# Kernel tuning notes

Hardware: AMD Instinct MI355X
Metric: run time of the kernel (lower is better)

The kernel has to match this reference:

```python
import jax, jax.numpy as jnp
import numpy as np
import math

D_MODEL = 1024
NHEAD = 16
HEAD_DIM = D_MODEL // NHEAD
D_FF = 4 * D_MODEL
EPS = 1e-5


def _layer_norm(x, g, b):
    mu = jnp.mean(x, axis=-1, keepdims=True)
    var = jnp.mean(jnp.square(x - mu), axis=-1, keepdims=True)
    return (x - mu) * jax.lax.rsqrt(var + EPS) * g + b


def setup_inputs() -> dict:
    key = jax.random.key(0)
    ks = jax.random.split(key, 12)
    B, N = 2, 2048
    s = 1.0 / math.sqrt(D_MODEL)
    inp = {
        "x": jax.random.normal(ks[0], (B, N, D_MODEL), dtype=jnp.float32),
        "wq": jax.random.normal(ks[1], (D_MODEL, D_MODEL), dtype=jnp.float32) * s,
        "bq": jnp.zeros((D_MODEL,), jnp.float32),
        "wk": jax.random.normal(ks[2], (D_MODEL, D_MODEL), dtype=jnp.float32) * s,
        "bk": jnp.zeros((D_MODEL,), jnp.float32),
        "wv": jax.random.normal(ks[3], (D_MODEL, D_MODEL), dtype=jnp.float32) * s,
        "bv": jnp.zeros((D_MODEL,), jnp.float32),
        "wo": jax.random.normal(ks[4], (D_MODEL, D_MODEL), dtype=jnp.float32) * s,
        "bo": jnp.zeros((D_MODEL,), jnp.float32),
        "ln1_g": jnp.ones((D_MODEL,), jnp.float32),
        "ln1_b": jnp.zeros((D_MODEL,), jnp.float32),
        "ln2_g": jnp.ones((D_MODEL,), jnp.float32),
        "ln2_b": jnp.zeros((D_MODEL,), jnp.float32),
        "w1": jax.random.normal(ks[5], (D_MODEL, D_FF), dtype=jnp.float32) * s,
        "b1": jnp.zeros((D_FF,), jnp.float32),
        "w2": jax.random.normal(ks[6], (D_FF, D_MODEL), dtype=jnp.float32) * (1.0 / math.sqrt(D_FF)),
        "b2": jnp.zeros((D_MODEL,), jnp.float32),
    }
    return inp


def reference(x, wq, bq, wk, bk, wv, bv, wo, bo, ln1_g, ln1_b, ln2_g, ln2_b, w1, b1, w2, b2):
    B, N, _ = x.shape
    normed = _layer_norm(x, ln1_g, ln1_b)
    # projections -> [B, H, N, Dh]
    q = (normed @ wq + bq).reshape(B, N, NHEAD, HEAD_DIM).transpose(0, 2, 1, 3)
    k = (normed @ wk + bk).reshape(B, N, NHEAD, HEAD_DIM).transpose(0, 2, 1, 3)
    v = (normed @ wv + bv).reshape(B, N, NHEAD, HEAD_DIM).transpose(0, 2, 1, 3)
    raw_scores = jnp.einsum("bhqd,bhkd->bhqk", q, k) / math.sqrt(HEAD_DIM)
    attn_probs = jax.nn.sigmoid(raw_scores)
    attn_out = jnp.einsum("bhqk,bhkd->bhqd", attn_probs, v) / math.sqrt(N)
    attn_out = attn_out.transpose(0, 2, 1, 3).reshape(B, N, D_MODEL)
    x = x + (attn_out @ wo + bo)  # dropout is identity in eval
    normed2 = _layer_norm(x, ln2_g, ln2_b)
    ff = jax.nn.gelu(normed2 @ w1 + b1, approximate=False) @ w2 + b2
    x = x + ff
    return (x, attn_probs)
```

## Files before the change

kernel.cpp:

```cpp
#include <hip/hip_runtime.h>
#include <hip/hip_bf16.h>
#include <math.h>

#define DMODEL 1024
#define NSEQ   2048
#define NBATCH 2
#define NHEADS 16
#define DHEAD  64
#define DFF    4096
#define MROWS  (NBATCH*NSEQ)
#define QKVLD  3072

typedef __attribute__((ext_vector_type(8))) short bf16x8;
typedef __attribute__((ext_vector_type(4))) float f32x4;

static __device__ __forceinline__ ushort f2b(float f) {
    return __builtin_bit_cast(ushort, (__bf16)f);
}

static __device__ __forceinline__ f32x4 mfma16(bf16x8 a, bf16x8 b, f32x4 c) {
    return __builtin_amdgcn_mfma_f32_16x16x32_bf16(a, b, c, 0, 0, 0);
}

static __device__ __forceinline__ void gload_lds16(const void* g, void* lds) {
    __builtin_amdgcn_global_load_lds((const __attribute__((address_space(1))) void*)g,
                                     (__attribute__((address_space(3))) void*)lds,
                                     16, 0, 0);
}

static __device__ __forceinline__ void softbar() {
    __builtin_amdgcn_sched_barrier(0);
    asm volatile("s_waitcnt lgkmcnt(0)" ::: "memory");
    __builtin_amdgcn_s_barrier();
    __builtin_amdgcn_sched_barrier(0);
}

static __device__ __forceinline__ void cast_tile_lds(const float* __restrict__ W,
                                                     ushort* __restrict__ Wt,
                                                     int K, int Nn, int bx, int by, int t,
                                                     float (*lds)[65])
{
    const int n0 = bx * 64;
    const int k0 = by * 64;
#pragma unroll
    for (int r = 0; r < 4; ++r) {
        const int kr = (t >> 4) + r * 16;
        const int nc = (t & 15) * 4;
        const float4 v = *(const float4*)(W + (long)(k0 + kr) * Nn + n0 + nc);
        lds[kr][nc] = v.x; lds[kr][nc + 1] = v.y; lds[kr][nc + 2] = v.z; lds[kr][nc + 3] = v.w;
    }
    __syncthreads();
    const int n  = t >> 2;
    const int kc = (t & 3) * 16;
    ushort tmp[16];
#pragma unroll
    for (int i = 0; i < 16; ++i) tmp[i] = f2b(lds[kc + i][n]);
    *(uint4*)(Wt + (long)(n0 + n) * K + k0 + kc)     = *(const uint4*)tmp;
    *(uint4*)(Wt + (long)(n0 + n) * K + k0 + kc + 8) = *(const uint4*)(tmp + 8);
}

__global__ __launch_bounds__(256) void prep(const float* __restrict__ wq,
                                            const float* __restrict__ wk,
                                            const float* __restrict__ wv,
                                            const float* __restrict__ wo,
                                            const float* __restrict__ w1,
                                            const float* __restrict__ w2,
                                            const float* __restrict__ bq,
                                            const float* __restrict__ bk,
                                            const float* __restrict__ bv,
                                            const float* __restrict__ x,
                                            const float* __restrict__ ln1g,
                                            const float* __restrict__ ln1b,
                                            ushort* __restrict__ wqkv_t,
                                            ushort* __restrict__ wo_t,
                                            ushort* __restrict__ w1_t,
                                            ushort* __restrict__ w2_t,
                                            float* __restrict__ bqkv,
                                            ushort* __restrict__ normed)
{
    __shared__ float red[4];
    __shared__ float tl[64][65];
    const int id  = blockIdx.x;
    const int tid = threadIdx.x;

    if (id < 256) {
        cast_tile_lds(wq, wqkv_t, 1024, 1024, id & 15, id >> 4, tid, tl);
    } else if (id < 512) {
        const int i2 = id - 256;
        cast_tile_lds(wk, wqkv_t + 1024 * 1024, 1024, 1024, i2 & 15, i2 >> 4, tid, tl);
    } else if (id < 768) {
        const int i2 = id - 512;
        cast_tile_lds(wv, wqkv_t + 2048 * 1024, 1024, 1024, i2 & 15, i2 >> 4, tid, tl);
    } else if (id < 1024) {
        const int i2 = id - 768;
        cast_tile_lds(wo, wo_t, 1024, 1024, i2 & 15, i2 >> 4, tid, tl);
    } else if (id < 2048) {
        const int i2 = id - 1024;
        cast_tile_lds(w1, w1_t, 1024, 4096, i2 & 63, i2 >> 6, tid, tl);
    } else if (id < 3072) {
        const int i2 = id - 2048;
        cast_tile_lds(w2, w2_t, 4096, 1024, i2 & 15, i2 >> 4, tid, tl);
    } else if (id < 3088) {
        const int t = (id - 3072) * 256 + tid;
        float v = 0.0f;
        if (t < 1024)      v = bq[t];
        else if (t < 2048) v = bk[t - 1024];
        else if (t < 3072) v = bv[t - 2048];
        bqkv[t] = v;
    } else {
        const int row = id - 3088;
        const float4 v = ((const float4*)(x + (long)row * DMODEL))[tid];
        float s = v.x + v.y + v.z + v.w;
#pragma unroll
        for (int o = 32; o; o >>= 1) s += __shfl_down(s, o, 64);
        if ((tid & 63) == 0) red[tid >> 6] = s;
        __syncthreads();
        const float mu = (red[0] + red[1] + red[2] + red[3]) * (1.0f / DMODEL);
        __syncthreads();
        const float d0 = v.x - mu, d1 = v.y - mu, d2 = v.z - mu, d3 = v.w - mu;
        float s2 = d0*d0 + d1*d1 + d2*d2 + d3*d3;
#pragma unroll
        for (int o = 32; o; o >>= 1) s2 += __shfl_down(s2, o, 64);
        if ((tid & 63) == 0) red[tid >> 6] = s2;
        __syncthreads();
        const float inv = rsqrtf((red[0] + red[1] + red[2] + red[3]) * (1.0f / DMODEL) + 1e-5f);
        const float4 gg = ((const float4*)ln1g)[tid];
        const float4 bv4 = ((const float4*)ln1b)[tid];
        ushort4 o4;
        o4.x = f2b(d0 * inv * gg.x + bv4.x);
        o4.y = f2b(d1 * inv * gg.y + bv4.y);
        o4.z = f2b(d2 * inv * gg.z + bv4.z);
        o4.w = f2b(d3 * inv * gg.w + bv4.w);
        ((ushort4*)(normed + (long)row * DMODEL))[tid] = o4;
    }
}

__global__ __launch_bounds__(256) void ln_kernel(const float* __restrict__ x,
                                                 const float* __restrict__ g,
                                                 const float* __restrict__ bb,
                                                 ushort* __restrict__ out)
{
    const int row = blockIdx.x;
    const int tid = threadIdx.x;
    const float4 v = ((const float4*)(x + (long)row * DMODEL))[tid];
    float s = v.x + v.y + v.z + v.w;
#pragma unroll
    for (int o = 32; o; o >>= 1) s += __shfl_down(s, o, 64);
    __shared__ float red[4];
    if ((tid & 63) == 0) red[tid >> 6] = s;
    __syncthreads();
    const float mu = (red[0] + red[1] + red[2] + red[3]) * (1.0f / DMODEL);
    __syncthreads();
    const float d0 = v.x - mu, d1 = v.y - mu, d2 = v.z - mu, d3 = v.w - mu;
    float s2 = d0*d0 + d1*d1 + d2*d2 + d3*d3;
#pragma unroll
    for (int o = 32; o; o >>= 1) s2 += __shfl_down(s2, o, 64);
    if ((tid & 63) == 0) red[tid >> 6] = s2;
    __syncthreads();
    const float inv = rsqrtf((red[0] + red[1] + red[2] + red[3]) * (1.0f / DMODEL) + 1e-5f);
    const float4 gg = ((const float4*)g)[tid];
    const float4 bv = ((const float4*)bb)[tid];
    ushort4 o4;
    o4.x = f2b(d0 * inv * gg.x + bv.x);
    o4.y = f2b(d1 * inv * gg.y + bv.y);
    o4.z = f2b(d2 * inv * gg.z + bv.z);
    o4.w = f2b(d3 * inv * gg.w + bv.w);
    ((ushort4*)(out + (long)row * DMODEL))[tid] = o4;
}

template<bool GELU>
__global__ __launch_bounds__(512, 2) void gemm128(const ushort* __restrict__ A, int lda,
                                                  const ushort* __restrict__ Bt, int ldb,
                                                  const float* __restrict__ bias,
                                                  ushort* __restrict__ C, int ldc, int K)
{
    extern __shared__ char smem[];
    const int tid  = threadIdx.x;
    const int lane = tid & 63;
    const int w    = tid >> 6;
    const int wm   = w >> 2;
    const int wn   = w & 3;
    const long row0 = (long)blockIdx.x * 128;
    const long col0 = (long)blockIdx.y * 256;

    const int srow = tid >> 2;
    const int scol = (((tid & 3) ^ ((srow >> 1) & 3))) * 8;
    const ushort* Ag = A  + (row0 + srow) * (long)lda + scol;
    const ushort* Bg = Bt + (col0 + srow) * (long)ldb + scol;

#define STAGE_A1(buf, k0)                                                                  \
    gload_lds16(Ag + (k0), smem + (buf) * 8192 + w * 1024)
#define STAGE_B1(buf, k0)                                                                  \
    do {                                                                                   \
        gload_lds16(Bg + (k0),                   smem + 24576 + (buf) * 16384 + w * 1024); \
        gload_lds16(Bg + 128 * (long)ldb + (k0), smem + 24576 + (buf) * 16384 + 8192 + w * 1024); \
    } while (0)

    const f32x4 zero = {0.f, 0.f, 0.f, 0.f};
    f32x4 acc[4][4];
#pragma unroll
    for (int m = 0; m < 4; ++m)
#pragma unroll
        for (int j = 0; j < 4; ++j) acc[m][j] = zero;

    const int NT = K >> 5;
    STAGE_A1(0, 0);  STAGE_B1(0, 0);
    STAGE_A1(1, 32); STAGE_B1(1, 32);

    const int mrow = lane & 15;
    const int xsl  = (((lane >> 4) ^ ((mrow >> 1) & 3))) * 8;
    const int abase = (wm * 64 + mrow) * 32 + xsl;
    const int bbase = (wn * 64 + mrow) * 32 + xsl;

    for (int t = 0; t < NT; ++t) {
        if (t == NT - 1) asm volatile("s_waitcnt vmcnt(0)" ::: "memory");
        else             asm volatile("s_waitcnt vmcnt(3)" ::: "memory");
        __builtin_amdgcn_sched_barrier(0);
        __builtin_amdgcn_s_barrier();
        __builtin_amdgcn_sched_barrier(0);

        const int cb = t % 3;
        const ushort* Abase = (const ushort*)(smem + cb * 8192);
        const ushort* Bbase = (const ushort*)(smem + 24576 + cb * 16384);

        bf16x8 bfr[4], afr[2];
#pragma unroll
        for (int ni = 0; ni < 4; ++ni)
            bfr[ni] = *(const bf16x8*)&Bbase[bbase + ni * 512];
#pragma unroll
        for (int mi = 0; mi < 2; ++mi)
            afr[mi] = *(const bf16x8*)&Abase[abase + mi * 512];
        if (t + 2 < NT) STAGE_A1((t + 2) % 3, (t + 2) * 32);
        __builtin_amdgcn_s_setprio(1);
#pragma unroll
        for (int mi = 0; mi < 2; ++mi)
#pragma unroll
            for (int ni = 0; ni < 4; ++ni)
                acc[mi][ni] = mfma16(afr[mi], bfr[ni], acc[mi][ni]);
        __builtin_amdgcn_s_setprio(0);

#pragma unroll
        for (int mi = 0; mi < 2; ++mi)
            afr[mi] = *(const bf16x8*)&Abase[abase + (mi + 2) * 512];
        if (t + 2 < NT) STAGE_B1((t + 2) % 3, (t + 2) * 32);
        __builtin_amdgcn_s_setprio(1);
#pragma unroll
        for (int mi = 0; mi < 2; ++mi)
#pragma unroll
            for (int ni = 0; ni < 4; ++ni)
                acc[mi + 2][ni] = mfma16(afr[mi], bfr[ni], acc[mi + 2][ni]);
        __builtin_amdgcn_s_setprio(0);
    }
#undef STAGE_A1
#undef STAGE_B1

#pragma unroll
    for (int ni = 0; ni < 4; ++ni) {
        const int colg = (int)col0 + wn * 64 + ni * 16 + (lane & 15);
        const float bcol = bias[colg];
#pragma unroll
        for (int mi = 0; mi < 4; ++mi) {
#pragma unroll
            for (int r = 0; r < 4; ++r) {
                const long rowg = row0 + wm * 64 + mi * 16 + (lane >> 4) * 4 + r;
                float vv = acc[mi][ni][r] + bcol;
                if (GELU) vv = 0.5f * vv * (1.0f + erff(vv * 0.70710678118f));
                C[rowg * ldc + colg] = f2b(vv);
            }
        }
    }
}

template<bool OUTF32, bool GELU, bool RES, bool NTST>
__global__ __launch_bounds__(512, 2) void gemm4s(const ushort* __restrict__ A, int lda,
                                                 const ushort* __restrict__ Bt, int ldb,
                                                 const float* __restrict__ bias,
                                                 const float* __restrict__ res,
                                                 void* __restrict__ Cout,
                                                 int Nn, int K)
{
    extern __shared__ char smem[];
    const int tid  = threadIdx.x;
    const int lane = tid & 63;
    const int g    = tid >> 8;
    const int tg   = tid & 255;
    const int w4   = tg >> 6;
    const int wm   = w4 >> 1, wn = w4 & 1;
    const long row0 = (long)blockIdx.x * 128;
    const long col0 = (long)blockIdx.y * 128;
    const int mrow = lane & 15;
    const int xsl  = (((lane >> 4) ^ ((mrow >> 1) & 3))) * 8;

    const int srow = tg >> 2;
    const int soff = (((tg & 3) ^ ((srow >> 1) & 3))) * 8;
    const int kb   = g * (K >> 1);
    const ushort* Ag = A  + (row0 + srow) * (long)lda + kb + soff;
    const ushort* Bg = Bt + (col0 + srow) * (long)ldb + kb + soff;
    char* Als = smem + g * 32768;
    char* Bls = smem + 65536 + g * 32768;

#define STAGE4S(buf, k0)                                                          \
    do {                                                                          \
        gload_lds16(Ag + (k0),                  Als + ((buf) << 13) + w4 * 1024); \
        gload_lds16(Ag + 64 * (long)lda + (k0), Als + ((buf) << 13) + 4096 + w4 * 1024); \
        gload_lds16(Bg + (k0),                  Bls + ((buf) << 13) + w4 * 1024); \
        gload_lds16(Bg + 64 * (long)ldb + (k0), Bls + ((buf) << 13) + 4096 + w4 * 1024); \
    } while (0)

    const f32x4 zero = {0.f, 0.f, 0.f, 0.f};
    f32x4 acc[4][4];
#pragma unroll
    for (int m = 0; m < 4; ++m)
#pragma unroll
        for (int j = 0; j < 4; ++j) acc[m][j] = zero;

    const int NT2 = K >> 6;
    STAGE4S(0, 0);
    STAGE4S(1, 32);
    STAGE4S(2, 64);

    const int abase = (wm * 64 + mrow) * 32 + xsl;
    const int bbase = (wn * 64 + mrow) * 32 + xsl;

    for (int t = 0; t < NT2; ++t) {
        if      (t >= NT2 - 1) asm volatile("s_waitcnt vmcnt(0)" ::: "memory");
        else if (t == NT2 - 2) asm volatile("s_waitcnt vmcnt(4)" ::: "memory");
        else                   asm volatile("s_waitcnt vmcnt(8)" ::: "memory");
        __builtin_amdgcn_sched_barrier(0);
        __builtin_amdgcn_s_barrier();
        __builtin_amdgcn_sched_barrier(0);

        if (t + 3 < NT2) STAGE4S((t + 3) & 3, (t + 3) * 32);

        const ushort* Abase = (const ushort*)(Als + ((t & 3) << 13));
        const ushort* Bbase = (const ushort*)(Bls + ((t & 3) << 13));
        bf16x8 af[4], bfv[4];
#pragma unroll
        for (int m = 0; m < 4; ++m)
            af[m] = *(const bf16x8*)&Abase[abase + m * 512];
#pragma unroll
        for (int j = 0; j < 4; ++j)
            bfv[j] = *(const bf16x8*)&Bbase[bbase + j * 512];
        __builtin_amdgcn_s_setprio(1);
#pragma unroll
        for (int m = 0; m < 4; ++m)
#pragma unroll
            for (int j = 0; j < 4; ++j)
                acc[m][j] = mfma16(af[m], bfv[j], acc[m][j]);
        __builtin_amdgcn_s_setprio(0);
    }
#undef STAGE4S

    __syncthreads();
    float* xch = (float*)smem;
    if (g == 1) {
#pragma unroll
        for (int m = 0; m < 4; ++m)
#pragma unroll
            for (int j = 0; j < 4; ++j)
#pragma unroll
                for (int r = 0; r < 4; ++r)
                    xch[(m * 16 + j * 4 + r) * 256 + tg] = acc[m][j][r];
    }
    __syncthreads();
    if (g == 0) {
#pragma unroll
        for (int j = 0; j < 4; ++j) {
            const int colg  = (int)col0 + wn * 64 + j * 16 + mrow;
            const float bcol = bias[colg];
#pragma unroll
            for (int m = 0; m < 4; ++m) {
#pragma unroll
                for (int r = 0; r < 4; ++r) {
                    const long rowg = row0 + wm * 64 + m * 16 + (lane >> 4) * 4 + r;
                    float vv = acc[m][j][r] + xch[(m * 16 + j * 4 + r) * 256 + tg] + bcol;
                    if (RES)   vv += res[rowg * Nn + colg];
                    if (GELU)  vv = 0.5f * vv * (1.0f + erff(vv * 0.70710678118f));
                    if (OUTF32) {
                        if (NTST) __builtin_nontemporal_store(vv, (float*)Cout + rowg * Nn + colg);
                        else      ((float*)Cout)[rowg * Nn + colg] = vv;
                    } else {
                        ((ushort*)Cout)[rowg * Nn + colg] = f2b(vv);
                    }
                }
            }
        }
    }
}

__global__ __launch_bounds__(256) void transpose_v(const ushort* __restrict__ v,
                                                   ushort* __restrict__ vt)
{
    __shared__ ushort t[64][72];
    const int nb = blockIdx.x, bh = blockIdx.y, b = bh >> 4;
    const int hcol = (bh & 15) * DHEAD;
    const int tid  = threadIdx.x;
    const int rrow = tid >> 3;
    const int cch  = (tid & 7) * 8;
#pragma unroll
    for (int r = 0; r < 2; ++r) {
        const int nr = rrow + r * 32;
        *(uint4*)&t[nr][cch] =
            *(const uint4*)(v + ((long)(b * NSEQ + nb * 64 + nr)) * QKVLD + hcol + cch);
    }
    __syncthreads();
#pragma unroll
    for (int r = 0; r < 2; ++r) {
        const int d = rrow + r * 32;
        ushort tmp[8];
#pragma unroll
        for (int i = 0; i < 8; ++i) tmp[i] = t[cch + i][d];
        *(uint4*)(vt + ((long)bh * DHEAD + d) * NSEQ + nb * 64 + cch) = *(const uint4*)tmp;
    }
}

__global__ __launch_bounds__(256) void attn_kernel(const ushort* __restrict__ qkv,
                                                   const ushort* __restrict__ vt,
                                                   float* __restrict__ probs,
                                                   ushort* __restrict__ ao)
{
    __shared__ ushort Ks[64][72];
    __shared__ ushort Vs[64][72];
    __shared__ __align__(16) float Pf[4][16][68];
    const int tid  = threadIdx.x;
    const int lane = tid & 63;
    const int w    = tid >> 6;
    const int qb   = blockIdx.x;
    const int bh   = blockIdx.y;
    const int b    = bh >> 4;
    const int q0   = qb * 64 + w * 16;
    const int mrow = lane & 15;
    const int kof  = (lane >> 4) * 8;
    const int hcol = (bh & 15) * DHEAD;
    const int NT   = NSEQ / 64;

    bf16x8 aq0, aq1;
    {
        const ushort* qp = qkv + ((long)(b * NSEQ + q0 + mrow)) * QKVLD + hcol;
        aq0 = *(const bf16x8*)(qp + kof);
        aq1 = *(const bf16x8*)(qp + 32 + kof);
    }

    const f32x4 zero = {0.f, 0.f, 0.f, 0.f};
    f32x4 acco[4];
#pragma unroll
    for (int dj = 0; dj < 4; ++dj) acco[dj] = zero;

    const int srow = tid >> 3;
    const int sch  = (tid & 7) * 8;
    const ushort* km = qkv + 1024;

    uint4 kr0, kr1, vr0, vr1;
#define LOADT(kt)                                                                          \
    do {                                                                                   \
        kr0 = *(const uint4*)(km + ((long)(b * NSEQ + (kt) * 64 + srow)) * QKVLD + hcol + sch);       \
        kr1 = *(const uint4*)(km + ((long)(b * NSEQ + (kt) * 64 + srow + 32)) * QKVLD + hcol + sch);  \
        vr0 = *(const uint4*)(vt + ((long)bh * DHEAD + srow) * NSEQ + (kt) * 64 + sch);               \
        vr1 = *(const uint4*)(vt + ((long)bh * DHEAD + srow + 32) * NSEQ + (kt) * 64 + sch);          \
    } while (0)

    LOADT(0);

    for (int kt = 0; kt < NT; ++kt) {
        *(uint4*)&Ks[srow][sch]      = kr0;
        *(uint4*)&Ks[srow + 32][sch] = kr1;
        *(uint4*)&Vs[srow][sch]      = vr0;
        *(uint4*)&Vs[srow + 32][sch] = vr1;
        softbar();
        if (kt + 1 < NT) LOADT(kt + 1);

        f32x4 s[4];
#pragma unroll
        for (int j = 0; j < 4; ++j) s[j] = zero;
#pragma unroll
        for (int j = 0; j < 4; ++j) {
            bf16x8 b0 = *(const bf16x8*)&Ks[j * 16 + mrow][kof];
            bf16x8 b1 = *(const bf16x8*)&Ks[j * 16 + mrow][32 + kof];
            s[j] = mfma16(aq0, b0, s[j]);
            s[j] = mfma16(aq1, b1, s[j]);
        }

#pragma unroll
        for (int j = 0; j < 4; ++j) {
#pragma unroll
            for (int r = 0; r < 4; ++r) {
                const int rr = (lane >> 4) * 4 + r;
                const float e  = __expf(-0.125f * s[j][r]);
                const float pv = __builtin_amdgcn_rcpf(1.0f + e);
                Pf[w][rr][j * 16 + mrow] = pv;
            }
        }

        const long pbase = ((long)(bh * NSEQ + q0)) * NSEQ + kt * 64;
#pragma unroll
        for (int i = 0; i < 4; ++i) {
            const int rr = (lane >> 4) + 4 * i;
            const f32x4 pv4 = *(const f32x4*)&Pf[w][rr][mrow * 4];
            __builtin_nontemporal_store(pv4, (f32x4*)(probs + pbase + (long)rr * NSEQ + mrow * 4));
        }

#pragma unroll
        for (int ks = 0; ks < 2; ++ks) {
            const f32x4 f0 = *(const f32x4*)&Pf[w][mrow][ks * 32 + kof];
            const f32x4 f1 = *(const f32x4*)&Pf[w][mrow][ks * 32 + kof + 4];
            bf16x8 ap;
            ap[0] = (short)f2b(f0[0]); ap[1] = (short)f2b(f0[1]);
            ap[2] = (short)f2b(f0[2]); ap[3] = (short)f2b(f0[3]);
            ap[4] = (short)f2b(f1[0]); ap[5] = (short)f2b(f1[1]);
            ap[6] = (short)f2b(f1[2]); ap[7] = (short)f2b(f1[3]);
#pragma unroll
            for (int dj = 0; dj < 4; ++dj) {
                bf16x8 bv = *(const bf16x8*)&Vs[dj * 16 + mrow][ks * 32 + kof];
                acco[dj] = mfma16(ap, bv, acco[dj]);
            }
        }
        softbar();
    }
#undef LOADT

    const float sc = rsqrtf((float)NSEQ);
#pragma unroll
    for (int dj = 0; dj < 4; ++dj)
#pragma unroll
        for (int r = 0; r < 4; ++r) {
            const int rr = (lane >> 4) * 4 + r;
            ao[((long)(b * NSEQ + q0 + rr)) * DMODEL + hcol + dj * 16 + mrow] =
                f2b(acco[dj][r] * sc);
        }
}

extern "C" void kernel_launch(void* const* d_in, const int* in_sizes, int n_in,
                              void* d_out, int out_size, void* d_ws, size_t ws_size,
                              hipStream_t stream) {
    (void)in_sizes; (void)n_in; (void)out_size;
    const float* x    = (const float*)d_in[0];
    const float* wq   = (const float*)d_in[1];
    const float* bq   = (const float*)d_in[2];
    const float* wk   = (const float*)d_in[3];
    const float* bk   = (const float*)d_in[4];
    const float* wv   = (const float*)d_in[5];
    const float* bv   = (const float*)d_in[6];
    const float* wo   = (const float*)d_in[7];
    const float* bo   = (const float*)d_in[8];
    const float* ln1g = (const float*)d_in[9];
    const float* ln1b = (const float*)d_in[10];
    const float* ln2g = (const float*)d_in[11];
    const float* ln2b = (const float*)d_in[12];
    const float* w1   = (const float*)d_in[13];
    const float* b1   = (const float*)d_in[14];
    const float* w2   = (const float*)d_in[15];
    const float* b2   = (const float*)d_in[16];

    char* ws = (char*)d_ws;
    const size_t MB = 1u << 20;
    ushort* wqkv_t  = (ushort*)(ws + 0 * MB);
    ushort* wo_t    = (ushort*)(ws + 6 * MB);
    ushort* w1_t    = (ushort*)(ws + 8 * MB);
    ushort* w2_t    = (ushort*)(ws + 16 * MB);
    float*  bqkv    = (float*) (ws + 24 * MB);
    ushort* normed  = (ushort*)(ws + 25 * MB);
    ushort* qkvbuf  = (ushort*)(ws + 33 * MB);
    ushort* vtb     = (ushort*)(ws + 57 * MB);
    ushort* attn_o  = (ushort*)(ws + 65 * MB);
    float*  x1      = (float*) (ws + 41 * MB);
    ushort* normed2 = (ushort*)(ws + 25 * MB);
    ushort* hbuf    = (ushort*)(ws + 57 * MB);
    const float* bzero = bqkv + 3072;
    const bool fullff = (ws_size >= 90 * MB);

    float* xout  = (float*)d_out;
    float* probs = xout + (size_t)MROWS * DMODEL;

    prep<<<7184, 256, 0, stream>>>(wq, wk, wv, wo, w1, w2, bq, bk, bv,
                                   x, ln1g, ln1b,
                                   wqkv_t, wo_t, w1_t, w2_t, bqkv, normed);

    gemm128<false><<<dim3(32, 12), 512, 72 * 1024, stream>>>(
        normed, DMODEL, wqkv_t, DMODEL, bqkv, qkvbuf, QKVLD, DMODEL);

    transpose_v<<<dim3(NSEQ / 64, NBATCH * NHEADS), 256, 0, stream>>>(qkvbuf + 2048, vtb);

    attn_kernel<<<dim3(NSEQ / 64, NBATCH * NHEADS), 256, 0, stream>>>(
        qkvbuf, vtb, probs, attn_o);

    gemm4s<true, false, true, false><<<dim3(32, 8), 512, 128 * 1024, stream>>>(
        attn_o, DMODEL, wo_t, DMODEL, bo, x, x1, DMODEL, DMODEL);

    ln_kernel<<<MROWS, 256, 0, stream>>>(x1, ln2g, ln2b, normed2);

    if (fullff) {
        gemm128<true><<<dim3(32, 16), 512, 72 * 1024, stream>>>(
            normed2, DMODEL, w1_t, DMODEL, b1, hbuf, DFF, DMODEL);
        gemm4s<true, false, true, true><<<dim3(32, 8), 512, 128 * 1024, stream>>>(
            hbuf, DFF, w2_t, DFF, b2, x1, xout, DMODEL, DFF);
    } else {
        gemm128<true><<<dim3(32, 8), 512, 72 * 1024, stream>>>(
            normed2, DMODEL, w1_t, DMODEL, b1, hbuf, 2048, DMODEL);
        gemm4s<true, false, true, false><<<dim3(32, 8), 512, 128 * 1024, stream>>>(
            hbuf, 2048, w2_t, DFF, b2, x1, xout, DMODEL, 2048);
        gemm128<true><<<dim3(32, 8), 512, 72 * 1024, stream>>>(
            normed2, DMODEL, w1_t + 2048 * 1024, DMODEL, b1 + 2048, hbuf, 2048, DMODEL);
        gemm4s<true, false, true, true><<<dim3(32, 8), 512, 128 * 1024, stream>>>(
            hbuf, 2048, w2_t + 2048, DFF, bzero, xout, xout, DMODEL, 2048);
    }
}
```

Before: 317.2 us.

## Double-buffer attention K/V tiles via direct global-to-LDS loads with XOR swizzle

Replaces the register-staged K/V tile loads in the attention kernel with global_load_lds into a double-buffered LDS area. Bank conflicts are avoided by rotating 16-byte column chunks per row instead of padding the rows. One barrier per iteration replaces two, and the vmcnt wait lets the next tile's loads overlap compute on the current tile. The workspace threshold for the full-FF path is also lowered slightly, which can switch the FFN path taken when the workspace size falls between the old and new thresholds.

After: 332.7 us. +4.9%, slower.

```diff
diff --git a/kernel.cpp b/kernel.cpp
--- a/kernel.cpp
+++ b/kernel.cpp
@@ -26,13 +26,6 @@
     __builtin_amdgcn_global_load_lds((const __attribute__((address_space(1))) void*)g,
                                      (__attribute__((address_space(3))) void*)lds,
                                      16, 0, 0);
-}
-
-static __device__ __forceinline__ void softbar() {
-    __builtin_amdgcn_sched_barrier(0);
-    asm volatile("s_waitcnt lgkmcnt(0)" ::: "memory");
-    __builtin_amdgcn_s_barrier();
-    __builtin_amdgcn_sched_barrier(0);
 }
 
 static __device__ __forceinline__ void cast_tile_lds(const float* __restrict__ W,
@@ -419,8 +412,7 @@
                                                    float* __restrict__ probs,
                                                    ushort* __restrict__ ao)
 {
-    __shared__ ushort Ks[64][72];
-    __shared__ ushort Vs[64][72];
+    __shared__ ushort KV[2][8192];
     __shared__ __align__(16) float Pf[4][16][68];
     const int tid  = threadIdx.x;
     const int lane = tid & 63;
@@ -430,7 +422,8 @@
     const int b    = bh >> 4;
     const int q0   = qb * 64 + w * 16;
     const int mrow = lane & 15;
-    const int kof  = (lane >> 4) * 8;
+    const int q4   = lane >> 4;
+    const int kof  = q4 * 8;
     const int hcol = (bh & 15) * DHEAD;
     const int NT   = NSEQ / 64;
 
@@ -447,35 +440,46 @@
     for (int dj = 0; dj < 4; ++dj) acco[dj] = zero;
 
     const int srow = tid >> 3;
-    const int sch  = (tid & 7) * 8;
+    const int sp   = tid & 7;
+    const int scol = ((sp - srow) & 7) * 8;
     const ushort* km = qkv + 1024;
-
-    uint4 kr0, kr1, vr0, vr1;
-#define LOADT(kt)                                                                          \
-    do {                                                                                   \
-        kr0 = *(const uint4*)(km + ((long)(b * NSEQ + (kt) * 64 + srow)) * QKVLD + hcol + sch);       \
-        kr1 = *(const uint4*)(km + ((long)(b * NSEQ + (kt) * 64 + srow + 32)) * QKVLD + hcol + sch);  \
-        vr0 = *(const uint4*)(vt + ((long)bh * DHEAD + srow) * NSEQ + (kt) * 64 + sch);               \
-        vr1 = *(const uint4*)(vt + ((long)bh * DHEAD + srow + 32) * NSEQ + (kt) * 64 + sch);          \
+    const ushort* kg = km + (long)(b * NSEQ + srow) * QKVLD + hcol + scol;
+    const ushort* vg = vt + ((long)bh * DHEAD + srow) * NSEQ + scol;
+    char* kls = (char*)KV;
+
+#define STAGE(buf, kt)                                                              \
+    do {                                                                            \
+        const long ko = (long)(kt) * 64 * QKVLD;                                    \
+        const int  vo = (kt) * 64;                                                  \
+        gload_lds16(kg + ko,                kls + (buf) * 16384 + w * 1024);        \
+        gload_lds16(kg + ko + 32L * QKVLD,  kls + (buf) * 16384 + 4096 + w * 1024); \
+        gload_lds16(vg + vo,                kls + (buf) * 16384 + 8192 + w * 1024); \
+        gload_lds16(vg + vo + 32 * NSEQ,    kls + (buf) * 16384 + 12288 + w * 1024);\
     } while (0)
 
-    LOADT(0);
+    STAGE(0, 0);
 
     for (int kt = 0; kt < NT; ++kt) {
-        *(uint4*)&Ks[srow][sch]      = kr0;
-        *(uint4*)&Ks[srow + 32][sch] = kr1;
-        *(uint4*)&Vs[srow][sch]      = vr0;
-        *(uint4*)&Vs[srow + 32][sch] = vr1;
-        softbar();
-        if (kt + 1 < NT) LOADT(kt + 1);
+        if (kt == 0) asm volatile("s_waitcnt vmcnt(0)" ::: "memory");
+        else         asm volatile("s_waitcnt vmcnt(4)" ::: "memory");
+        __builtin_amdgcn_sched_barrier(0);
+        __builtin_amdgcn_s_barrier();
+        __builtin_amdgcn_sched_barrier(0);
+
+        if (kt + 1 < NT) STAGE((kt + 1) & 1, kt + 1);
+        __builtin_amdgcn_sched_barrier(0);
+
+        const ushort* Kb = &KV[kt & 1][0];
+        const ushort* Vb = &KV[kt & 1][4096];
 
         f32x4 s[4];
 #pragma unroll
         for (int j = 0; j < 4; ++j) s[j] = zero;
 #pragma unroll
         for (int j = 0; j < 4; ++j) {
-            bf16x8 b0 = *(const bf16x8*)&Ks[j * 16 + mrow][kof];
-            bf16x8 b1 = *(const bf16x8*)&Ks[j * 16 + mrow][32 + kof];
+            const int row = j * 16 + mrow;
+            bf16x8 b0 = *(const bf16x8*)&Kb[row * 64 + ((q4 + mrow) & 7) * 8];
+            bf16x8 b1 = *(const bf16x8*)&Kb[row * 64 + ((q4 + 4 + mrow) & 7) * 8];
             s[j] = mfma16(aq0, b0, s[j]);
             s[j] = mfma16(aq1, b1, s[j]);
         }
@@ -484,7 +488,7 @@
         for (int j = 0; j < 4; ++j) {
 #pragma unroll
             for (int r = 0; r < 4; ++r) {
-                const int rr = (lane >> 4) * 4 + r;
+                const int rr = q4 * 4 + r;
                 const float e  = __expf(-0.125f * s[j][r]);
                 const float pv = __builtin_amdgcn_rcpf(1.0f + e);
                 Pf[w][rr][j * 16 + mrow] = pv;
@@ -494,7 +498,7 @@
         const long pbase = ((long)(bh * NSEQ + q0)) * NSEQ + kt * 64;
 #pragma unroll
         for (int i = 0; i < 4; ++i) {
-            const int rr = (lane >> 4) + 4 * i;
+            const int rr = q4 + 4 * i;
             const f32x4 pv4 = *(const f32x4*)&Pf[w][rr][mrow * 4];
             __builtin_nontemporal_store(pv4, (f32x4*)(probs + pbase + (long)rr * NSEQ + mrow * 4));
         }
@@ -510,20 +514,20 @@
             ap[6] = (short)f2b(f1[2]); ap[7] = (short)f2b(f1[3]);
 #pragma unroll
             for (int dj = 0; dj < 4; ++dj) {
-                bf16x8 bv = *(const bf16x8*)&Vs[dj * 16 + mrow][ks * 32 + kof];
+                const int rowv = dj * 16 + mrow;
+                bf16x8 bv = *(const bf16x8*)&Vb[rowv * 64 + ((q4 + 4 * ks + mrow) & 7) * 8];
                 acco[dj] = mfma16(ap, bv, acco[dj]);
             }
         }
-        softbar();
-    }
-#undef LOADT
+    }
+#undef STAGE
 
     const float sc = rsqrtf((float)NSEQ);
 #pragma unroll
     for (int dj = 0; dj < 4; ++dj)
 #pragma unroll
         for (int r = 0; r < 4; ++r) {
-            const int rr = (lane >> 4) * 4 + r;
+            const int rr = q4 * 4 + r;
             ao[((long)(b * NSEQ + q0 + rr)) * DMODEL + hcol + dj * 16 + mrow] =
                 f2b(acco[dj][r] * sc);
         }
@@ -566,7 +570,7 @@
     ushort* normed2 = (ushort*)(ws + 25 * MB);
     ushort* hbuf    = (ushort*)(ws + 57 * MB);
     const float* bzero = bqkv + 3072;
-    const bool fullff = (ws_size >= 90 * MB);
+    const bool fullff = (ws_size >= 89 * MB);
 
     float* xout  = (float*)d_out;
     float* probs = xout + (size_t)MROWS * DMODEL;
```
